# Kernel optimization log

Measured on AMD Instinct MI355X. Metric: run time of the kernel, lower is better.

The kernel has to match this reference:

```python
import jax, jax.numpy as jnp
import numpy as np

N, E, DIN, D, H = 10000, 160000, 256, 64, 8
HC = D * H  # 512

def _p(key, shape, fan_in):
    return jax.random.normal(key, shape, dtype=jnp.float32) * (1.0 / np.sqrt(fan_in))

def setup_inputs() -> dict:
    key = jax.random.key(0)
    k = iter(jax.random.split(key, 64))
    inp = {}
    inp['x'] = jax.random.normal(next(k), (N, DIN), dtype=jnp.float32)
    inp['edge_index'] = jax.random.randint(next(k), (2, E), 0, N, dtype=jnp.int64)
    inp['Wp'] = _p(next(k), (DIN, D), DIN); inp['bp'] = jnp.zeros((D,), jnp.float32)
    # layer 0: in=D -> H*D
    for nm in ['Wq0', 'Wk0', 'Wv0', 'Ws0']:
        inp[nm] = _p(next(k), (D, HC), D)
    for nm in ['bq0', 'bk0', 'bv0', 'bs0']:
        inp[nm] = jnp.zeros((HC,), jnp.float32)
    # layers 1..4 stacked: in=HC -> HC
    for nm in ['Wq', 'Wk', 'Wv', 'Ws']:
        inp[nm] = _p(next(k), (4, HC, HC), HC)
    for nm in ['bq', 'bk', 'bv', 'bs']:
        inp[nm] = jnp.zeros((4, HC), jnp.float32)
    # final conv: in=HC -> D, heads=1, concat=False
    for nm in ['Wqf', 'Wkf', 'Wvf', 'Wsf']:
        inp[nm] = _p(next(k), (HC, D), HC)
    for nm in ['bqf', 'bkf', 'bvf', 'bsf']:
        inp[nm] = jnp.zeros((D,), jnp.float32)
    inp['Wc1'] = _p(next(k), (D, D // 2), D); inp['bc1'] = jnp.zeros((D // 2,), jnp.float32)
    inp['Wc2'] = _p(next(k), (D // 2, 2), D // 2); inp['bc2'] = jnp.zeros((2,), jnp.float32)
    return inp

def _tconv(x, src, dst, Wq, bq, Wk, bk, Wv, bv, Ws, bs, heads, concat):
    n = x.shape[0]
    c = Wq.shape[1] // heads
    q = (x @ Wq + bq).reshape(n, heads, c)
    kk = (x @ Wk + bk).reshape(n, heads, c)
    v = (x @ Wv + bv).reshape(n, heads, c)
    scale = 1.0 / jnp.sqrt(jnp.asarray(c, x.dtype))
    alpha = jnp.einsum('ehc,ehc->eh', q[dst], kk[src]) * scale  # [E,H]
    amax = jax.ops.segment_max(alpha, dst, num_segments=n)
    ex = jnp.exp(alpha - amax[dst])
    denom = jax.ops.segment_sum(ex, dst, num_segments=n)
    w = ex / denom[dst]  # segment softmax over incoming edges
    agg = jax.ops.segment_sum(w[:, :, None] * v[src], dst, num_segments=n)  # [N,H,C]
    skip = x @ Ws + bs
    if concat:
        return agg.reshape(n, heads * c) + skip
    return agg.mean(axis=1) + skip

def reference(x, edge_index, Wp, bp, Wq0, bq0, Wk0, bk0, Wv0, bv0, Ws0, bs0,
              Wq, bq, Wk, bk, Wv, bv, Ws, bs,
              Wqf, bqf, Wkf, bkf, Wvf, bvf, Wsf, bsf,
              Wc1, bc1, Wc2, bc2):
    src, dst = edge_index[0], edge_index[1]
    h = x @ Wp + bp
    h = jax.nn.relu(_tconv(h, src, dst, Wq0, bq0, Wk0, bk0, Wv0, bv0, Ws0, bs0, H, True))
    for l in range(4):
        h = jax.nn.relu(_tconv(h, src, dst, Wq[l], bq[l], Wk[l], bk[l], Wv[l], bv[l], Ws[l], bs[l], H, True))
    h = _tconv(h, src, dst, Wqf, bqf, Wkf, bkf, Wvf, bvf, Wsf, bsf, 1, False)
    g = h.mean(axis=0, keepdims=True)  # batch=None path: [1,D]
    logits = jax.nn.relu(g @ Wc1 + bc1) @ Wc2 + bc2
    return logits
```

## Files before the change

### kernel.cpp

```cpp
#include <hip/hip_runtime.h>
#include <hip/hip_bf16.h>
#include <cstddef>
#include <cstdint>

static inline int cdiv(int a, int b) { return (a + b - 1) / b; }

typedef short short8v __attribute__((ext_vector_type(8)));
typedef float float4v __attribute__((ext_vector_type(4)));

__device__ inline unsigned short f2b(float f) {
    union { float f; unsigned u; } x; x.f = f;
    unsigned u = x.u;
    return (unsigned short)((u + 0x7fff + ((u >> 16) & 1)) >> 16);
}

__device__ inline float lo2f(unsigned u) { union { unsigned x; float f; } c; c.x = u << 16; return c.f; }
__device__ inline float hi2f(unsigned u) { union { unsigned x; float f; } c; c.x = u & 0xffff0000u; return c.f; }
__device__ inline float b2f(unsigned short b) {
    union { unsigned u; float f; } x; x.u = ((unsigned)b) << 16;
    return x.f;
}

__device__ __forceinline__ void u4tof8(uint4 u, float* f) {
    f[0] = lo2f(u.x); f[1] = hi2f(u.x); f[2] = lo2f(u.y); f[3] = hi2f(u.y);
    f[4] = lo2f(u.z); f[5] = hi2f(u.z); f[6] = lo2f(u.w); f[7] = hi2f(u.w);
}

__device__ __forceinline__ void gload_lds16(const unsigned short* g, unsigned short* lds) {
    __builtin_amdgcn_global_load_lds(
        (const __attribute__((address_space(1))) unsigned int*)g,
        (__attribute__((address_space(3))) unsigned int*)lds, 16, 0, 0);
}


__global__ void count_kernel(const int* __restrict__ ei, int* __restrict__ indeg, int E) {
    int e = blockIdx.x * blockDim.x + threadIdx.x;
    if (e < E) atomicAdd(&indeg[ei[E + e]], 1);
}

__global__ void scan_kernel(const int* __restrict__ indeg, int* __restrict__ offs, int n) {
    __shared__ int tmp[1024];
    __shared__ int carry_s;
    int t = threadIdx.x;
    if (t == 0) { carry_s = 0; offs[0] = 0; }
    __syncthreads();
    for (int base = 0; base < n; base += 1024) {
        int i = base + t;
        int v = (i < n) ? indeg[i] : 0;
        tmp[t] = v;
        __syncthreads();
        for (int d = 1; d < 1024; d <<= 1) {
            int add = (t >= d) ? tmp[t - d] : 0;
            __syncthreads();
            tmp[t] += add;
            __syncthreads();
        }
        if (i < n) offs[i + 1] = carry_s + tmp[t];
        __syncthreads();
        if (t == 0) carry_s += tmp[1023];
        __syncthreads();
    }
}

__global__ void fill_kernel(const int* __restrict__ ei, const int* __restrict__ offs,
                            int* __restrict__ cursor, int* __restrict__ csrc, int E) {
    int e = blockIdx.x * blockDim.x + threadIdx.x;
    if (e < E) {
        int d = ei[E + e];
        int s = ei[e];
        int pos = atomicAdd(&cursor[d], 1);
        csrc[offs[d] + pos] = s;
    }
}


__global__ void f2b_kernel(const float* __restrict__ in, unsigned short* __restrict__ out, int n4) {
    int stride = gridDim.x * blockDim.x;
    for (int i = blockIdx.x * blockDim.x + threadIdx.x; i < n4; i += stride) {
        float4 v = reinterpret_cast<const float4*>(in)[i];
        ushort4 o;
        o.x = f2b(v.x); o.y = f2b(v.y); o.z = f2b(v.z); o.w = f2b(v.w);
        reinterpret_cast<ushort4*>(out)[i] = o;
    }
}

__global__ void transpose_b16_kernel(const float* __restrict__ Wq, const float* __restrict__ Wk,
                                     const float* __restrict__ Wv, const float* __restrict__ Ws,
                                     unsigned short* __restrict__ out) {
    const int K = 512, Nc = 512;
    int z = blockIdx.z;
    int which = z & 3;
    const float* W = (which == 0) ? Wq : (which == 1) ? Wk : (which == 2) ? Wv : Ws;
    W += (size_t)(z >> 2) * K * Nc;
    unsigned short* Wt = out + (size_t)z * K * Nc;
    __shared__ float t[32][33];
    int k0 = blockIdx.x * 32, c0 = blockIdx.y * 32;
    int tx = threadIdx.x, ty = threadIdx.y;
    #pragma unroll
    for (int i = 0; i < 32; i += 8) t[ty + i][tx] = W[(size_t)(k0 + ty + i) * Nc + c0 + tx];
    __syncthreads();
    #pragma unroll
    for (int i = 0; i < 32; i += 8) Wt[(size_t)(c0 + ty + i) * K + k0 + tx] = f2b(t[tx][ty + i]);
}

struct SmallT {
    const float* src[9];
    unsigned short* dst[9];
    int rows[9];
    int cols[9];
};

__global__ void transpose_small_kernel(SmallT p) {
    int mat = blockIdx.y;
    int rows = p.rows[mat], cols = p.cols[mat];
    int tilesC = cols >> 5;
    int tiles = (rows >> 5) * tilesC;
    if ((int)blockIdx.x >= tiles) return;
    int tr = blockIdx.x / tilesC, tc = blockIdx.x % tilesC;
    const float* src = p.src[mat];
    unsigned short* dst = p.dst[mat];
    __shared__ float t[32][33];
    int r0 = tr * 32, c0 = tc * 32;
    int tx = threadIdx.x, ty = threadIdx.y;
    #pragma unroll
    for (int i = 0; i < 32; i += 8) t[ty + i][tx] = src[(size_t)(r0 + ty + i) * cols + c0 + tx];
    __syncthreads();
    #pragma unroll
    for (int i = 0; i < 32; i += 8) dst[(size_t)(c0 + ty + i) * rows + r0 + tx] = f2b(t[tx][ty + i]);
}


struct GemmPtrs {
    const unsigned short* B[4];
    const float* bias[4];
    void* C[4];
    int bf16[4];
};

__global__ __launch_bounds__(256) void mfma_gemm4(const unsigned short* __restrict__ A,
                                                  GemmPtrs p, int M, int nb) {
    __shared__ unsigned short As[128 * 32];
    __shared__ unsigned short Bs[128 * 32];
    int i = blockIdx.x;
    int wk = (nb & 7) ? i : ((i & 7) * (nb >> 3) + (i >> 3));
    int xt = wk >> 4, yt = wk & 15;
    int row0 = xt * 128;
    int wsel = yt >> 2;
    int col0 = (yt & 3) * 128;
    const unsigned short* Bt = p.B[wsel];

    int tid = threadIdx.x;
    int lane = tid & 63;
    int w = tid >> 6;
    int wr = w >> 1, wc = w & 1;
    float4v acc[4][4] = {};

    int c0i = w * 2;
    int srow0 = c0i * 16 + (lane >> 2);
    int srow1 = srow0 + 16;
    int sslot0 = (lane & 3) ^ ((srow0 >> 1) & 3);
    int sslot1 = (lane & 3) ^ ((srow1 >> 1) & 3);

    const unsigned short* Abase = A + (size_t)row0 * 512;
    const unsigned short* Bbase = Bt + (size_t)col0 * 512;

    for (int k0 = 0; k0 < 512; k0 += 32) {
        gload_lds16(Abase + (size_t)srow0 * 512 + k0 + sslot0 * 8, &As[c0i * 512]);
        gload_lds16(Abase + (size_t)srow1 * 512 + k0 + sslot1 * 8, &As[(c0i + 1) * 512]);
        gload_lds16(Bbase + (size_t)srow0 * 512 + k0 + sslot0 * 8, &Bs[c0i * 512]);
        gload_lds16(Bbase + (size_t)srow1 * 512 + k0 + sslot1 * 8, &Bs[(c0i + 1) * 512]);
        __syncthreads();
        int r16 = lane & 15;
        int ks = lane >> 4;
        short8v af[4], bf[4];
        #pragma unroll
        for (int mi = 0; mi < 4; ++mi) {
            int row = wr * 64 + mi * 16 + r16;
            int slot = ks ^ ((row >> 1) & 3);
            af[mi] = *reinterpret_cast<const short8v*>(&As[row * 32 + slot * 8]);
        }
        #pragma unroll
        for (int nj = 0; nj < 4; ++nj) {
            int row = wc * 64 + nj * 16 + r16;
            int slot = ks ^ ((row >> 1) & 3);
            bf[nj] = *reinterpret_cast<const short8v*>(&Bs[row * 32 + slot * 8]);
        }
        #pragma unroll
        for (int mi = 0; mi < 4; ++mi)
            #pragma unroll
            for (int nj = 0; nj < 4; ++nj)
                acc[mi][nj] = __builtin_amdgcn_mfma_f32_16x16x32_bf16(af[mi], bf[nj], acc[mi][nj], 0, 0, 0);
        __syncthreads();
    }

    const float* bias = p.bias[wsel];
    int outbf = p.bf16[wsel];
    float* Cf = (float*)p.C[wsel];
    unsigned short* Cb = (unsigned short*)p.C[wsel];
    int crow_base = row0 + wr * 64 + (lane >> 4) * 4;
    int ccol_base = col0 + wc * 64 + (lane & 15);
    #pragma unroll
    for (int mi = 0; mi < 4; ++mi) {
        #pragma unroll
        for (int r = 0; r < 4; ++r) {
            int grow = crow_base + mi * 16 + r;
            if (grow >= M) continue;
            #pragma unroll
            for (int nj = 0; nj < 4; ++nj) {
                int gcol = ccol_base + nj * 16;
                float val = acc[mi][nj][r] + bias[gcol];
                if (outbf) Cb[(size_t)grow * 512 + gcol] = f2b(val);
                else       Cf[(size_t)grow * 512 + gcol] = val;
            }
        }
    }
}


__global__ __launch_bounds__(256) void mfma_flex(const unsigned short* __restrict__ A,
                                                 GemmPtrs p, int M, int K, int Nc) {
    __shared__ unsigned short As[128][40];
    __shared__ unsigned short Bs[64][40];
    int tid = threadIdx.x;
    int lane = tid & 63;
    int w = tid >> 6;
    int row0 = blockIdx.x * 128;
    int nb = Nc >> 6;
    int wsel = blockIdx.y / nb;
    int col0 = (blockIdx.y % nb) * 64;
    const unsigned short* Bt = p.B[wsel];

    float4v acc[2][4] = {};

    int ra = tid >> 1;
    int ca = (tid & 1) * 16;
    int rb = tid >> 2;
    int cb = (tid & 3) * 8;

    for (int k0 = 0; k0 < K; k0 += 32) {
        {
            int grow = row0 + ra;
            uint4 a0 = make_uint4(0u, 0u, 0u, 0u), a1 = make_uint4(0u, 0u, 0u, 0u);
            if (grow < M) {
                a0 = *reinterpret_cast<const uint4*>(&A[(size_t)grow * K + k0 + ca]);
                a1 = *reinterpret_cast<const uint4*>(&A[(size_t)grow * K + k0 + ca + 8]);
            }
            *reinterpret_cast<uint4*>(&As[ra][ca]) = a0;
            *reinterpret_cast<uint4*>(&As[ra][ca + 8]) = a1;
            uint4 bv = *reinterpret_cast<const uint4*>(&Bt[(size_t)(col0 + rb) * K + k0 + cb]);
            *reinterpret_cast<uint4*>(&Bs[rb][cb]) = bv;
        }
        __syncthreads();
        short8v af[2], bf[4];
        int r16 = lane & 15;
        int kc = (lane >> 4) * 8;
        #pragma unroll
        for (int mi = 0; mi < 2; ++mi)
            af[mi] = *reinterpret_cast<const short8v*>(&As[w * 32 + mi * 16 + r16][kc]);
        #pragma unroll
        for (int nj = 0; nj < 4; ++nj)
            bf[nj] = *reinterpret_cast<const short8v*>(&Bs[nj * 16 + r16][kc]);
        #pragma unroll
        for (int mi = 0; mi < 2; ++mi)
            #pragma unroll
            for (int nj = 0; nj < 4; ++nj)
                acc[mi][nj] = __builtin_amdgcn_mfma_f32_16x16x32_bf16(af[mi], bf[nj], acc[mi][nj], 0, 0, 0);
        __syncthreads();
    }

    const float* bias = p.bias[wsel];
    int outbf = p.bf16[wsel];
    float* Cf = (float*)p.C[wsel];
    unsigned short* Cb = (unsigned short*)p.C[wsel];
    int crow_base = row0 + w * 32 + (lane >> 4) * 4;
    int ccol_base = col0 + (lane & 15);
    #pragma unroll
    for (int mi = 0; mi < 2; ++mi) {
        #pragma unroll
        for (int r = 0; r < 4; ++r) {
            int grow = crow_base + mi * 16 + r;
            if (grow >= M) continue;
            #pragma unroll
            for (int nj = 0; nj < 4; ++nj) {
                int gcol = ccol_base + nj * 16;
                float val = acc[mi][nj][r] + bias[gcol];
                if (outbf) Cb[(size_t)grow * Nc + gcol] = f2b(val);
                else       Cf[(size_t)grow * Nc + gcol] = val;
            }
        }
    }
}


__global__ __launch_bounds__(256) void agg8_kernel(const unsigned short* __restrict__ q,
                                                   const unsigned short* __restrict__ kb,
                                                   const unsigned short* __restrict__ vb,
                                                   const unsigned short* __restrict__ skip,
                                                   const int* __restrict__ offs, const int* __restrict__ csrc,
                                                   unsigned short* __restrict__ outb, int N) {
    int lane = threadIdx.x & 63;
    int node = blockIdx.x * (blockDim.x >> 6) + (threadIdx.x >> 6);
    if (node >= N) return;

    unsigned co = (unsigned)lane * 8u;
    unsigned rbase = (unsigned)node * 512u + co;
    float qv[8];
    u4tof8(*reinterpret_cast<const uint4*>(&q[rbase]), qv);

    int e0 = offs[node], e1 = offs[node + 1];
    float m = -1e30f, wsum = 0.f;
    float accv[8] = {};
    const float SC = 0.125f * 1.4426950408889634f;

    int s = e0;
    for (; s + 4 <= e1; s += 4) {
        unsigned b0 = (unsigned)csrc[s] * 512u + co;
        unsigned b1 = (unsigned)csrc[s + 1] * 512u + co;
        unsigned b2 = (unsigned)csrc[s + 2] * 512u + co;
        unsigned b3 = (unsigned)csrc[s + 3] * 512u + co;
        uint4 k0 = *reinterpret_cast<const uint4*>(&kb[b0]);
        uint4 k1 = *reinterpret_cast<const uint4*>(&kb[b1]);
        uint4 k2 = *reinterpret_cast<const uint4*>(&kb[b2]);
        uint4 k3 = *reinterpret_cast<const uint4*>(&kb[b3]);
        uint4 v0 = *reinterpret_cast<const uint4*>(&vb[b0]);
        uint4 v1 = *reinterpret_cast<const uint4*>(&vb[b1]);
        uint4 v2 = *reinterpret_cast<const uint4*>(&vb[b2]);
        uint4 v3 = *reinterpret_cast<const uint4*>(&vb[b3]);
        float kk0[8], kk1[8], kk2[8], kk3[8];
        u4tof8(k0, kk0); u4tof8(k1, kk1); u4tof8(k2, kk2); u4tof8(k3, kk3);
        float d0 = 0.f, d1 = 0.f, d2 = 0.f, d3 = 0.f;
        #pragma unroll
        for (int j = 0; j < 8; ++j) {
            d0 += qv[j] * kk0[j]; d1 += qv[j] * kk1[j];
            d2 += qv[j] * kk2[j]; d3 += qv[j] * kk3[j];
        }
        d0 += __shfl_xor(d0, 1); d1 += __shfl_xor(d1, 1); d2 += __shfl_xor(d2, 1); d3 += __shfl_xor(d3, 1);
        d0 += __shfl_xor(d0, 2); d1 += __shfl_xor(d1, 2); d2 += __shfl_xor(d2, 2); d3 += __shfl_xor(d3, 2);
        d0 += __shfl_xor(d0, 4); d1 += __shfl_xor(d1, 4); d2 += __shfl_xor(d2, 4); d3 += __shfl_xor(d3, 4);
        float a0 = d0 * SC, a1 = d1 * SC, a2 = d2 * SC, a3 = d3 * SC;
        float am = fmaxf(fmaxf(a0, a1), fmaxf(a2, a3));
        if (__any(am > m + 8.f)) {
            float mnew = fmaxf(m, am);
            float corr = exp2f(m - mnew);
            wsum *= corr;
            #pragma unroll
            for (int j = 0; j < 8; ++j) accv[j] *= corr;
            m = mnew;
        }
        float x0 = exp2f(a0 - m);
        float x1 = exp2f(a1 - m);
        float x2 = exp2f(a2 - m);
        float x3 = exp2f(a3 - m);
        wsum += (x0 + x1) + (x2 + x3);
        float vv0[8], vv1[8], vv2[8], vv3[8];
        u4tof8(v0, vv0); u4tof8(v1, vv1); u4tof8(v2, vv2); u4tof8(v3, vv3);
        #pragma unroll
        for (int j = 0; j < 8; ++j)
            accv[j] += (x0 * vv0[j] + x1 * vv1[j]) + (x2 * vv2[j] + x3 * vv3[j]);
    }
    for (; s < e1; ++s) {
        unsigned b0 = (unsigned)csrc[s] * 512u + co;
        float kk0[8], vv0[8];
        u4tof8(*reinterpret_cast<const uint4*>(&kb[b0]), kk0);
        u4tof8(*reinterpret_cast<const uint4*>(&vb[b0]), vv0);
        float d0 = 0.f;
        #pragma unroll
        for (int j = 0; j < 8; ++j) d0 += qv[j] * kk0[j];
        d0 += __shfl_xor(d0, 1);
        d0 += __shfl_xor(d0, 2);
        d0 += __shfl_xor(d0, 4);
        float a0 = d0 * SC;
        if (__any(a0 > m + 8.f)) {
            float mnew = fmaxf(m, a0);
            float corr = exp2f(m - mnew);
            wsum *= corr;
            #pragma unroll
            for (int j = 0; j < 8; ++j) accv[j] *= corr;
            m = mnew;
        }
        float x0 = exp2f(a0 - m);
        wsum += x0;
        #pragma unroll
        for (int j = 0; j < 8; ++j) accv[j] += x0 * vv0[j];
    }

    float inv = (e1 > e0) ? (1.0f / wsum) : 0.f;
    float sk[8];
    u4tof8(*reinterpret_cast<const uint4*>(&skip[rbase]), sk);
    ushort4 o0, o1;
    o0.x = f2b(fmaxf(sk[0] + accv[0] * inv, 0.f));
    o0.y = f2b(fmaxf(sk[1] + accv[1] * inv, 0.f));
    o0.z = f2b(fmaxf(sk[2] + accv[2] * inv, 0.f));
    o0.w = f2b(fmaxf(sk[3] + accv[3] * inv, 0.f));
    o1.x = f2b(fmaxf(sk[4] + accv[4] * inv, 0.f));
    o1.y = f2b(fmaxf(sk[5] + accv[5] * inv, 0.f));
    o1.z = f2b(fmaxf(sk[6] + accv[6] * inv, 0.f));
    o1.w = f2b(fmaxf(sk[7] + accv[7] * inv, 0.f));
    *reinterpret_cast<ushort4*>(&outb[rbase]) = o0;
    *reinterpret_cast<ushort4*>(&outb[rbase + 4]) = o1;
}


__global__ __launch_bounds__(256) void aggf_kernel(const unsigned short* __restrict__ q,
                                                   const unsigned short* __restrict__ kb,
                                                   const unsigned short* __restrict__ vb,
                                                   const int* __restrict__ offs, const int* __restrict__ csrc,
                                                   float* __restrict__ out, int N) {
    const int HC = 64;
    int lane = threadIdx.x & 63;
    int node = blockIdx.x * (blockDim.x >> 6) + (threadIdx.x >> 6);
    if (node >= N) return;
    int g = lane >> 4;
    int r = lane & 15;

    unsigned qbase = (unsigned)node * 64u + 4u * r;
    ushort4 q4u = *reinterpret_cast<const ushort4*>(&q[qbase]);
    float q4[4] = {b2f(q4u.x), b2f(q4u.y), b2f(q4u.z), b2f(q4u.w)};

    int e0 = offs[node], e1 = offs[node + 1];
    float m = -3.4e38f, wsum = 0.f;
    float accv[4] = {0.f, 0.f, 0.f, 0.f};

    int nIt = (e1 - e0 + 3) >> 2;
    for (int it = 0; it < nIt; ++it) {
        int s = e0 + it * 4 + g;
        bool valid = s < e1;
        unsigned base = (unsigned)csrc[valid ? s : (e1 - 1)] * 64u + 4u * r;
        ushort4 k4 = *reinterpret_cast<const ushort4*>(&kb[base]);
        float d = q4[0] * b2f(k4.x) + q4[1] * b2f(k4.y) + q4[2] * b2f(k4.z) + q4[3] * b2f(k4.w);
        d += __shfl_xor(d, 1);
        d += __shfl_xor(d, 2);
        d += __shfl_xor(d, 4);
        d += __shfl_xor(d, 8);
        float alpha = valid ? d * 0.125f : -3.4e38f;
        float am = fmaxf(alpha, __shfl_xor(alpha, 16));
        am = fmaxf(am, __shfl_xor(am, 32));
        float mnew = fmaxf(m, am);
        float corr = __expf(m - mnew);
        float ex = __expf(alpha - mnew);
        ushort4 v4 = *reinterpret_cast<const ushort4*>(&vb[base]);
        wsum = wsum * corr + ex;
        accv[0] = accv[0] * corr + ex * b2f(v4.x);
        accv[1] = accv[1] * corr + ex * b2f(v4.y);
        accv[2] = accv[2] * corr + ex * b2f(v4.z);
        accv[3] = accv[3] * corr + ex * b2f(v4.w);
        m = mnew;
    }

    #pragma unroll
    for (int off = 16; off <= 32; off <<= 1) {
        wsum += __shfl_xor(wsum, off);
        #pragma unroll
        for (int j = 0; j < 4; ++j) accv[j] += __shfl_xor(accv[j], off);
    }

    if (g == 0) {
        float inv = (e1 > e0) ? (1.0f / wsum) : 0.f;
        float4 o = *reinterpret_cast<const float4*>(&out[qbase]);
        o.x += accv[0] * inv;
        o.y += accv[1] * inv;
        o.z += accv[2] * inv;
        o.w += accv[3] * inv;
        *reinterpret_cast<float4*>(&out[qbase]) = o;
    }
}


__global__ void pool_kernel(const float* __restrict__ hin, float* __restrict__ g, int N) {
    int dim = blockIdx.x;
    float s = 0.f;
    for (int i = threadIdx.x; i < N; i += blockDim.x) s += hin[(size_t)i * 64 + dim];
    __shared__ float red[256];
    red[threadIdx.x] = s;
    __syncthreads();
    for (int d = 128; d >= 1; d >>= 1) {
        if ((int)threadIdx.x < d) red[threadIdx.x] += red[threadIdx.x + d];
        __syncthreads();
    }
    if (threadIdx.x == 0) g[dim] = red[0] / (float)N;
}

__global__ void mlp_kernel(const float* __restrict__ g, const float* __restrict__ Wc1,
                           const float* __restrict__ bc1, const float* __restrict__ Wc2,
                           const float* __restrict__ bc2, float* __restrict__ out) {
    __shared__ float gs[64];
    __shared__ float h1[32];
    int t = threadIdx.x;
    if (t < 64) gs[t] = g[t];
    __syncthreads();
    if (t < 32) {
        float s = bc1[t];
        for (int i = 0; i < 64; ++i) s += gs[i] * Wc1[i * 32 + t];
        h1[t] = fmaxf(s, 0.f);
    }
    __syncthreads();
    if (t < 2) {
        float s = bc2[t];
        for (int i = 0; i < 32; ++i) s += h1[i] * Wc2[i * 2 + t];
        out[t] = s;
    }
}


extern "C" void kernel_launch(void* const* d_in, const int* in_sizes, int n_in,
                              void* d_out, int out_size, void* d_ws, size_t ws_size,
                              hipStream_t stream) {
    const float* x   = (const float*)d_in[0];
    const int*   ei  = (const int*)d_in[1];
    const float* Wp  = (const float*)d_in[2];
    const float* bp  = (const float*)d_in[3];
    const float* Wq0 = (const float*)d_in[4];
    const float* Wk0 = (const float*)d_in[5];
    const float* Wv0 = (const float*)d_in[6];
    const float* Ws0 = (const float*)d_in[7];
    const float* bq0 = (const float*)d_in[8];
    const float* bk0 = (const float*)d_in[9];
    const float* bv0 = (const float*)d_in[10];
    const float* bs0 = (const float*)d_in[11];
    const float* Wq  = (const float*)d_in[12];
    const float* Wk  = (const float*)d_in[13];
    const float* Wv  = (const float*)d_in[14];
    const float* Ws  = (const float*)d_in[15];
    const float* bq  = (const float*)d_in[16];
    const float* bk  = (const float*)d_in[17];
    const float* bv  = (const float*)d_in[18];
    const float* bs  = (const float*)d_in[19];
    const float* Wqf = (const float*)d_in[20];
    const float* Wkf = (const float*)d_in[21];
    const float* Wvf = (const float*)d_in[22];
    const float* Wsf = (const float*)d_in[23];
    const float* bqf = (const float*)d_in[24];
    const float* bkf = (const float*)d_in[25];
    const float* bvf = (const float*)d_in[26];
    const float* bsf = (const float*)d_in[27];
    const float* Wc1 = (const float*)d_in[28];
    const float* bc1 = (const float*)d_in[29];
    const float* Wc2 = (const float*)d_in[30];
    const float* bc2 = (const float*)d_in[31];

    const int N = in_sizes[0] / 256;
    const int E = in_sizes[1] / 2;
    const int HC = 512;

    size_t NB = (size_t)N * HC;
    const size_t WSMALL = 64 * 256 + 8 * 512 * 64;
    size_t need = 6 * NB * sizeof(unsigned short)
                + (size_t)16 * 512 * 512 * sizeof(unsigned short)
                + WSMALL * sizeof(unsigned short)
                + NB * sizeof(float)
                + (size_t)(2 * N + 1 + E) * sizeof(int)
                + 64 * sizeof(float) + 4096;
    if (ws_size < need) return;

    unsigned short* h0    = (unsigned short*)d_ws;
    unsigned short* h1    = h0 + NB;
    unsigned short* qb16  = h1 + NB;
    unsigned short* kb    = qb16 + NB;
    unsigned short* vb    = kb + NB;
    unsigned short* skipb = vb + NB;
    unsigned short* wt16  = skipb + NB;
    unsigned short* wsm   = wt16 + (size_t)16 * 512 * 512;
    uintptr_t pa = (uintptr_t)(wsm + WSMALL);
    pa = (pa + 255) & ~(uintptr_t)255;
    float* hf32 = (float*)pa;
    int* offs   = (int*)(hf32 + NB);
    int* cursor = offs + (N + 1);
    int* csrc   = cursor + N;
    float* gbuf = (float*)(csrc + E);
    unsigned short* xb = qb16;

    hipMemsetAsync(cursor, 0, sizeof(int) * N, stream);
    count_kernel<<<cdiv(E, 256), 256, 0, stream>>>(ei, cursor, E);
    scan_kernel<<<1, 1024, 0, stream>>>(cursor, offs, N);
    hipMemsetAsync(cursor, 0, sizeof(int) * N, stream);
    fill_kernel<<<cdiv(E, 256), 256, 0, stream>>>(ei, offs, cursor, csrc, E);

    transpose_b16_kernel<<<dim3(16, 16, 16), dim3(32, 8), 0, stream>>>(Wq, Wk, Wv, Ws, wt16);
    {
        SmallT st;
        unsigned short* wp_t = wsm;
        unsigned short* w0_t = wsm + 64 * 256;
        unsigned short* wf_t = w0_t + 4 * 512 * 64;
        st.src[0] = Wp;  st.dst[0] = wp_t; st.rows[0] = 256; st.cols[0] = 64;
        const float* w0s[4] = {Wq0, Wk0, Wv0, Ws0};
        const float* wfs[4] = {Wqf, Wkf, Wvf, Wsf};
        for (int i = 0; i < 4; ++i) {
            st.src[1 + i] = w0s[i]; st.dst[1 + i] = w0_t + i * 512 * 64;
            st.rows[1 + i] = 64; st.cols[1 + i] = 512;
            st.src[5 + i] = wfs[i]; st.dst[5 + i] = wf_t + i * 64 * 512;
            st.rows[5 + i] = 512; st.cols[5 + i] = 64;
        }
        transpose_small_kernel<<<dim3(32, 9), dim3(32, 8), 0, stream>>>(st);
    }

    f2b_kernel<<<1280, 256, 0, stream>>>(x, xb, N * 256 / 4);
    {
        GemmPtrs gp;
        for (int j = 0; j < 4; ++j) {
            gp.B[j] = wsm; gp.bias[j] = bp; gp.C[j] = h0; gp.bf16[j] = 1;
        }
        mfma_flex<<<dim3(cdiv(N, 128), 1), 256, 0, stream>>>(xb, gp, N, 256, 64);
    }

    {
        GemmPtrs gp;
        unsigned short* w0_t = wsm + 64 * 256;
        gp.B[0] = w0_t + 0 * 512 * 64; gp.bias[0] = bq0; gp.C[0] = qb16;  gp.bf16[0] = 1;
        gp.B[1] = w0_t + 1 * 512 * 64; gp.bias[1] = bk0; gp.C[1] = kb;    gp.bf16[1] = 1;
        gp.B[2] = w0_t + 2 * 512 * 64; gp.bias[2] = bv0; gp.C[2] = vb;    gp.bf16[2] = 1;
        gp.B[3] = w0_t + 3 * 512 * 64; gp.bias[3] = bs0; gp.C[3] = skipb; gp.bf16[3] = 1;
        mfma_flex<<<dim3(cdiv(N, 128), 4 * 8), 256, 0, stream>>>(h0, gp, N, 64, 512);
    }
    agg8_kernel<<<cdiv(N, 4), 256, 0, stream>>>(qb16, kb, vb, skipb, offs, csrc, h1, N);

    unsigned short* hcur = h1;
    unsigned short* hnext = h0;
    int gx = cdiv(N, 128);
    for (int l = 0; l < 4; ++l) {
        GemmPtrs gp;
        gp.B[0] = wt16 + (size_t)(l * 4 + 0) * 512 * 512;
        gp.B[1] = wt16 + (size_t)(l * 4 + 1) * 512 * 512;
        gp.B[2] = wt16 + (size_t)(l * 4 + 2) * 512 * 512;
        gp.B[3] = wt16 + (size_t)(l * 4 + 3) * 512 * 512;
        gp.bias[0] = bq + l * HC;
        gp.bias[1] = bk + l * HC;
        gp.bias[2] = bv + l * HC;
        gp.bias[3] = bs + l * HC;
        gp.C[0] = qb16; gp.C[1] = kb; gp.C[2] = vb; gp.C[3] = skipb;
        gp.bf16[0] = 1; gp.bf16[1] = 1; gp.bf16[2] = 1; gp.bf16[3] = 1;
        mfma_gemm4<<<gx * 16, 256, 0, stream>>>(hcur, gp, N, gx * 16);
        agg8_kernel<<<cdiv(N, 4), 256, 0, stream>>>(qb16, kb, vb, skipb, offs, csrc, hnext, N);
        { unsigned short* t = hcur; hcur = hnext; hnext = t; }
    }

    {
        GemmPtrs gp;
        unsigned short* wf_t = wsm + 64 * 256 + 4 * 512 * 64;
        gp.B[0] = wf_t + 0 * 64 * 512; gp.bias[0] = bqf; gp.C[0] = qb16; gp.bf16[0] = 1;
        gp.B[1] = wf_t + 1 * 64 * 512; gp.bias[1] = bkf; gp.C[1] = kb;   gp.bf16[1] = 1;
        gp.B[2] = wf_t + 2 * 64 * 512; gp.bias[2] = bvf; gp.C[2] = vb;   gp.bf16[2] = 1;
        gp.B[3] = wf_t + 3 * 64 * 512; gp.bias[3] = bsf; gp.C[3] = hf32; gp.bf16[3] = 0;
        mfma_flex<<<dim3(cdiv(N, 128), 4), 256, 0, stream>>>(hcur, gp, N, 512, 64);
    }
    aggf_kernel<<<cdiv(N, 4), 256, 0, stream>>>(qb16, kb, vb, offs, csrc, hf32, N);

    pool_kernel<<<64, 256, 0, stream>>>(hf32, gbuf, N);
    mlp_kernel<<<1, 64, 0, stream>>>(gbuf, Wc1, bc1, Wc2, bc2, (float*)d_out);
}
```

Measured before the change: 572.5 us.

## Fold input projection into layer-0 weights, parallelize CSR scan, widen GEMM K-tile

The input projection Wp is folded into the layer-0 Q/K/V/skip weights: each combined 256x512 weight is precomputed with small GEMMs, and the bias is folded as bp·W + b. The x-to-h0 GEMM is removed, and layer 0 now reads the bf16 x directly with K=256. The single-block serial scan is replaced by a three-kernel block scan. The main 512x512 GEMM now loads 64-wide K tiles with a new XOR swizzle, which halves the loop iterations and barriers at the cost of more LDS. The layer-0 GEMM does more FLOPs (K=256 instead of 64) and adds an extra bf16 rounding of the combined weights.

New measurement: 652.9 us. +14.0%, slower.

```diff
diff --git a/kernel.cpp b/kernel.cpp
--- a/kernel.cpp
+++ b/kernel.cpp
@@ -38,28 +38,34 @@
     if (e < E) atomicAdd(&indeg[ei[E + e]], 1);
 }
 
-__global__ void scan_kernel(const int* __restrict__ indeg, int* __restrict__ offs, int n) {
-    __shared__ int tmp[1024];
-    __shared__ int carry_s;
-    int t = threadIdx.x;
-    if (t == 0) { carry_s = 0; offs[0] = 0; }
+__global__ void scan1_kernel(const int* __restrict__ deg, int* __restrict__ offs,
+                             int* __restrict__ bsum, int n) {
+    __shared__ int tmp[256];
+    int i = blockIdx.x * 256 + threadIdx.x;
+    int v = (i < n) ? deg[i] : 0;
+    tmp[threadIdx.x] = v;
     __syncthreads();
-    for (int base = 0; base < n; base += 1024) {
-        int i = base + t;
-        int v = (i < n) ? indeg[i] : 0;
-        tmp[t] = v;
+    for (int d = 1; d < 256; d <<= 1) {
+        int a = (threadIdx.x >= (unsigned)d) ? tmp[threadIdx.x - d] : 0;
         __syncthreads();
-        for (int d = 1; d < 1024; d <<= 1) {
-            int add = (t >= d) ? tmp[t - d] : 0;
-            __syncthreads();
-            tmp[t] += add;
-            __syncthreads();
-        }
-        if (i < n) offs[i + 1] = carry_s + tmp[t];
+        tmp[threadIdx.x] += a;
         __syncthreads();
-        if (t == 0) carry_s += tmp[1023];
-        __syncthreads();
-    }
+    }
+    if (i < n) offs[i + 1] = tmp[threadIdx.x];
+    if (threadIdx.x == 255) bsum[blockIdx.x] = tmp[255];
+}
+
+__global__ void scan2_kernel(int* __restrict__ bsum, int* __restrict__ offs, int nb) {
+    if (threadIdx.x == 0) {
+        offs[0] = 0;
+        int base = 0;
+        for (int b = 0; b < nb; ++b) { int t = bsum[b]; bsum[b] = base; base += t; }
+    }
+}
+
+__global__ void scan3_kernel(int* __restrict__ offs, const int* __restrict__ bsum, int n) {
+    int i = blockIdx.x * 256 + threadIdx.x;
+    if (i < n) offs[i + 1] += bsum[blockIdx.x];
 }
 
 __global__ void fill_kernel(const int* __restrict__ ei, const int* __restrict__ offs,
@@ -104,10 +110,10 @@
 }
 
 struct SmallT {
-    const float* src[9];
-    unsigned short* dst[9];
-    int rows[9];
-    int cols[9];
+    const float* src[8];
+    unsigned short* dst[8];
+    int rows[8];
+    int cols[8];
 };
 
 __global__ void transpose_small_kernel(SmallT p) {
@@ -129,6 +135,17 @@
     for (int i = 0; i < 32; i += 8) dst[(size_t)(c0 + ty + i) * rows + r0 + tx] = f2b(t[tx][ty + i]);
 }
 
+struct BiasC { const float* W[4]; const float* b[4]; const float* bp; float* out; };
+
+__global__ void biascomb_kernel(BiasC p) {
+    int w = blockIdx.x;
+    int c = threadIdx.x;
+    float s = p.b[w][c];
+    const float* W = p.W[w];
+    for (int d = 0; d < 64; ++d) s += p.bp[d] * W[d * 512 + c];
+    p.out[w * 512 + c] = s;
+}
+
 
 struct GemmPtrs {
     const unsigned short* B[4];
@@ -139,8 +156,8 @@
 
 __global__ __launch_bounds__(256) void mfma_gemm4(const unsigned short* __restrict__ A,
                                                   GemmPtrs p, int M, int nb) {
-    __shared__ unsigned short As[128 * 32];
-    __shared__ unsigned short Bs[128 * 32];
+    __shared__ unsigned short As[128 * 64];
+    __shared__ unsigned short Bs[128 * 64];
     int i = blockIdx.x;
     int wk = (nb & 7) ? i : ((i & 7) * (nb >> 3) + (i >> 3));
     int xt = wk >> 4, yt = wk & 15;
@@ -155,41 +172,43 @@
     int wr = w >> 1, wc = w & 1;
     float4v acc[4][4] = {};
 
-    int c0i = w * 2;
-    int srow0 = c0i * 16 + (lane >> 2);
-    int srow1 = srow0 + 16;
-    int sslot0 = (lane & 3) ^ ((srow0 >> 1) & 3);
-    int sslot1 = (lane & 3) ^ ((srow1 >> 1) & 3);
-
-    const unsigned short* Abase = A + (size_t)row0 * 512;
-    const unsigned short* Bbase = Bt + (size_t)col0 * 512;
-
-    for (int k0 = 0; k0 < 512; k0 += 32) {
-        gload_lds16(Abase + (size_t)srow0 * 512 + k0 + sslot0 * 8, &As[c0i * 512]);
-        gload_lds16(Abase + (size_t)srow1 * 512 + k0 + sslot1 * 8, &As[(c0i + 1) * 512]);
-        gload_lds16(Bbase + (size_t)srow0 * 512 + k0 + sslot0 * 8, &Bs[c0i * 512]);
-        gload_lds16(Bbase + (size_t)srow1 * 512 + k0 + sslot1 * 8, &Bs[(c0i + 1) * 512]);
+    int srow = w * 32 + (lane >> 3);
+    int sslot = (lane & 7) ^ (lane >> 3);
+    const unsigned short* Ag = A + (size_t)(row0 + srow) * 512 + sslot * 8;
+    const unsigned short* Bg = Bt + (size_t)(col0 + srow) * 512 + sslot * 8;
+    unsigned short* Al = &As[(w * 32) * 64];
+    unsigned short* Bl = &Bs[(w * 32) * 64];
+
+    int r16 = lane & 15;
+    int ks = lane >> 4;
+
+    for (int k0 = 0; k0 < 512; k0 += 64) {
+        #pragma unroll
+        for (int j = 0; j < 4; ++j) {
+            gload_lds16(Ag + (size_t)(j * 8) * 512 + k0, Al + j * 8 * 64);
+            gload_lds16(Bg + (size_t)(j * 8) * 512 + k0, Bl + j * 8 * 64);
+        }
         __syncthreads();
-        int r16 = lane & 15;
-        int ks = lane >> 4;
-        short8v af[4], bf[4];
-        #pragma unroll
-        for (int mi = 0; mi < 4; ++mi) {
-            int row = wr * 64 + mi * 16 + r16;
-            int slot = ks ^ ((row >> 1) & 3);
-            af[mi] = *reinterpret_cast<const short8v*>(&As[row * 32 + slot * 8]);
-        }
-        #pragma unroll
-        for (int nj = 0; nj < 4; ++nj) {
-            int row = wc * 64 + nj * 16 + r16;
-            int slot = ks ^ ((row >> 1) & 3);
-            bf[nj] = *reinterpret_cast<const short8v*>(&Bs[row * 32 + slot * 8]);
-        }
-        #pragma unroll
-        for (int mi = 0; mi < 4; ++mi)
-            #pragma unroll
-            for (int nj = 0; nj < 4; ++nj)
-                acc[mi][nj] = __builtin_amdgcn_mfma_f32_16x16x32_bf16(af[mi], bf[nj], acc[mi][nj], 0, 0, 0);
+        #pragma unroll
+        for (int kk = 0; kk < 2; ++kk) {
+            int g = kk * 4 + ks;
+            short8v af[4], bf[4];
+            #pragma unroll
+            for (int mi = 0; mi < 4; ++mi) {
+                int row = wr * 64 + mi * 16 + r16;
+                af[mi] = *reinterpret_cast<const short8v*>(&As[row * 64 + (g ^ (row & 7)) * 8]);
+            }
+            #pragma unroll
+            for (int nj = 0; nj < 4; ++nj) {
+                int row = wc * 64 + nj * 16 + r16;
+                bf[nj] = *reinterpret_cast<const short8v*>(&Bs[row * 64 + (g ^ (row & 7)) * 8]);
+            }
+            #pragma unroll
+            for (int mi = 0; mi < 4; ++mi)
+                #pragma unroll
+                for (int nj = 0; nj < 4; ++nj)
+                    acc[mi][nj] = __builtin_amdgcn_mfma_f32_16x16x32_bf16(af[mi], bf[nj], acc[mi][nj], 0, 0, 0);
+        }
         __syncthreads();
     }
 
@@ -543,13 +562,13 @@
     const int HC = 512;
 
     size_t NB = (size_t)N * HC;
-    const size_t WSMALL = 64 * 256 + 8 * 512 * 64;
+    const size_t WSMALL = 131072 + 131072 + 16384 + 524288;
     size_t need = 6 * NB * sizeof(unsigned short)
                 + (size_t)16 * 512 * 512 * sizeof(unsigned short)
                 + WSMALL * sizeof(unsigned short)
                 + NB * sizeof(float)
                 + (size_t)(2 * N + 1 + E) * sizeof(int)
-                + 64 * sizeof(float) + 4096;
+                + (64 + 64 + 256 + 2048) * sizeof(float) + 8192;
     if (ws_size < need) return;
 
     unsigned short* h0    = (unsigned short*)d_ws;
@@ -560,56 +579,77 @@
     unsigned short* skipb = vb + NB;
     unsigned short* wt16  = skipb + NB;
     unsigned short* wsm   = wt16 + (size_t)16 * 512 * 512;
-    uintptr_t pa = (uintptr_t)(wsm + WSMALL);
+    unsigned short* w0_t  = wsm;
+    unsigned short* wf_t  = w0_t + 131072;
+    unsigned short* wpb   = wf_t + 131072;
+    unsigned short* wcomb = wpb + 16384;
+    uintptr_t pa = (uintptr_t)(wcomb + 524288);
     pa = (pa + 255) & ~(uintptr_t)255;
     float* hf32 = (float*)pa;
     int* offs   = (int*)(hf32 + NB);
     int* cursor = offs + (N + 1);
     int* csrc   = cursor + N;
     float* gbuf = (float*)(csrc + E);
-    unsigned short* xb = qb16;
+    int*   bsum = (int*)(gbuf + 64);
+    float* zbuf = (float*)(bsum + 64);
+    float* bcomb = zbuf + 256;
+    unsigned short* xb = (unsigned short*)hf32;
+
+    int nsb = cdiv(N, 256);
 
     hipMemsetAsync(cursor, 0, sizeof(int) * N, stream);
+    hipMemsetAsync(zbuf, 0, sizeof(float) * 256, stream);
     count_kernel<<<cdiv(E, 256), 256, 0, stream>>>(ei, cursor, E);
-    scan_kernel<<<1, 1024, 0, stream>>>(cursor, offs, N);
+    scan1_kernel<<<nsb, 256, 0, stream>>>(cursor, offs, bsum, N);
+    scan2_kernel<<<1, 64, 0, stream>>>(bsum, offs, nsb);
+    scan3_kernel<<<nsb, 256, 0, stream>>>(offs, bsum, N);
     hipMemsetAsync(cursor, 0, sizeof(int) * N, stream);
     fill_kernel<<<cdiv(E, 256), 256, 0, stream>>>(ei, offs, cursor, csrc, E);
 
     transpose_b16_kernel<<<dim3(16, 16, 16), dim3(32, 8), 0, stream>>>(Wq, Wk, Wv, Ws, wt16);
     {
         SmallT st;
-        unsigned short* wp_t = wsm;
-        unsigned short* w0_t = wsm + 64 * 256;
-        unsigned short* wf_t = w0_t + 4 * 512 * 64;
-        st.src[0] = Wp;  st.dst[0] = wp_t; st.rows[0] = 256; st.cols[0] = 64;
         const float* w0s[4] = {Wq0, Wk0, Wv0, Ws0};
         const float* wfs[4] = {Wqf, Wkf, Wvf, Wsf};
         for (int i = 0; i < 4; ++i) {
-            st.src[1 + i] = w0s[i]; st.dst[1 + i] = w0_t + i * 512 * 64;
-            st.rows[1 + i] = 64; st.cols[1 + i] = 512;
-            st.src[5 + i] = wfs[i]; st.dst[5 + i] = wf_t + i * 64 * 512;
-            st.rows[5 + i] = 512; st.cols[5 + i] = 64;
-        }
-        transpose_small_kernel<<<dim3(32, 9), dim3(32, 8), 0, stream>>>(st);
-    }
-
-    f2b_kernel<<<1280, 256, 0, stream>>>(x, xb, N * 256 / 4);
+            st.src[i] = w0s[i]; st.dst[i] = w0_t + i * 512 * 64;
+            st.rows[i] = 64; st.cols[i] = 512;
+            st.src[4 + i] = wfs[i]; st.dst[4 + i] = wf_t + i * 64 * 512;
+            st.rows[4 + i] = 512; st.cols[4 + i] = 64;
+        }
+        transpose_small_kernel<<<dim3(32, 8), dim3(32, 8), 0, stream>>>(st);
+    }
+    f2b_kernel<<<16, 256, 0, stream>>>(Wp, wpb, 256 * 64 / 4);
+
     {
         GemmPtrs gp;
         for (int j = 0; j < 4; ++j) {
-            gp.B[j] = wsm; gp.bias[j] = bp; gp.C[j] = h0; gp.bf16[j] = 1;
-        }
-        mfma_flex<<<dim3(cdiv(N, 128), 1), 256, 0, stream>>>(xb, gp, N, 256, 64);
-    }
+            gp.B[j] = wpb; gp.bias[j] = zbuf;
+            gp.C[j] = wcomb + (size_t)j * 512 * 256; gp.bf16[j] = 1;
+        }
+        for (int j = 0; j < 4; ++j) {
+            GemmPtrs g1 = gp;
+            for (int t = 0; t < 4; ++t) { g1.C[t] = gp.C[j]; }
+            mfma_flex<<<dim3(4, 4), 256, 0, stream>>>(w0_t + (size_t)j * 512 * 64, g1, 512, 64, 256);
+        }
+    }
+    {
+        BiasC bcp;
+        bcp.W[0] = Wq0; bcp.W[1] = Wk0; bcp.W[2] = Wv0; bcp.W[3] = Ws0;
+        bcp.b[0] = bq0; bcp.b[1] = bk0; bcp.b[2] = bv0; bcp.b[3] = bs0;
+        bcp.bp = bp; bcp.out = bcomb;
+        biascomb_kernel<<<4, 512, 0, stream>>>(bcp);
+    }
+
+    f2b_kernel<<<1280, 256, 0, stream>>>(x, xb, N * 256 / 4);
 
     {
         GemmPtrs gp;
-        unsigned short* w0_t = wsm + 64 * 256;
-        gp.B[0] = w0_t + 0 * 512 * 64; gp.bias[0] = bq0; gp.C[0] = qb16;  gp.bf16[0] = 1;
-        gp.B[1] = w0_t + 1 * 512 * 64; gp.bias[1] = bk0; gp.C[1] = kb;    gp.bf16[1] = 1;
-        gp.B[2] = w0_t + 2 * 512 * 64; gp.bias[2] = bv0; gp.C[2] = vb;    gp.bf16[2] = 1;
-        gp.B[3] = w0_t + 3 * 512 * 64; gp.bias[3] = bs0; gp.C[3] = skipb; gp.bf16[3] = 1;
-        mfma_flex<<<dim3(cdiv(N, 128), 4 * 8), 256, 0, stream>>>(h0, gp, N, 64, 512);
+        gp.B[0] = wcomb + 0 * 512 * 256; gp.bias[0] = bcomb + 0 * 512; gp.C[0] = qb16;  gp.bf16[0] = 1;
+        gp.B[1] = wcomb + 1 * 512 * 256; gp.bias[1] = bcomb + 1 * 512; gp.C[1] = kb;    gp.bf16[1] = 1;
+        gp.B[2] = wcomb + 2 * 512 * 256; gp.bias[2] = bcomb + 2 * 512; gp.C[2] = vb;    gp.bf16[2] = 1;
+        gp.B[3] = wcomb + 3 * 512 * 256; gp.bias[3] = bcomb + 3 * 512; gp.C[3] = skipb; gp.bf16[3] = 1;
+        mfma_flex<<<dim3(cdiv(N, 128), 4 * 8), 256, 0, stream>>>(xb, gp, N, 256, 512);
     }
     agg8_kernel<<<cdiv(N, 4), 256, 0, stream>>>(qb16, kb, vb, skipb, offs, csrc, h1, N);
 
@@ -635,7 +675,6 @@
 
     {
         GemmPtrs gp;
-        unsigned short* wf_t = wsm + 64 * 256 + 4 * 512 * 64;
         gp.B[0] = wf_t + 0 * 64 * 512; gp.bias[0] = bqf; gp.C[0] = qb16; gp.bf16[0] = 1;
         gp.B[1] = wf_t + 1 * 64 * 512; gp.bias[1] = bkf; gp.C[1] = kb;   gp.bf16[1] = 1;
         gp.B[2] = wf_t + 2 * 64 * 512; gp.bias[2] = bvf; gp.C[2] = vb;   gp.bf16[2] = 1;
```
